# Performance work log

Hardware: AMD Instinct MI355X
Metric: run time of the kernel (lower is better)

The kernel has to match this reference:

```python
import jax, jax.numpy as jnp
import numpy as np

S = 2048   # seq_len
E = 1024   # embed_dim
N = 16     # num_heads
H = 64     # head_dim
CL = 1024  # context_length (sliding window)
BASE = 10000.0


def _rope(x, positions, base=BASE):
    # x: (seq, heads, head_dim); even/odd interleaved rotation per RotaryEmbedding
    hd = x.shape[-1]
    dim = hd // 2
    freqs = jnp.exp(-jnp.arange(dim, dtype=x.dtype) * (np.log(base) / dim))
    angles = positions.astype(x.dtype)[:, None] * freqs[None, :]  # (seq, dim)
    cos = jnp.cos(angles)[:, None, :]
    sin = jnp.sin(angles)[:, None, :]
    xe = x[..., ::2]
    xo = x[..., 1::2]
    re = xe * cos - xo * sin
    ro = xe * sin + xo * cos
    return jnp.zeros_like(x).at[..., ::2].set(re).at[..., 1::2].set(ro)


def setup_inputs() -> dict:
    key = jax.random.key(0)
    ks = jax.random.split(key, 9)
    scale = 1.0 / np.sqrt(E)  # keep logits O(1) like eqx.nn.Linear init
    x = jax.random.normal(ks[0], (S, E), jnp.float32)
    Wq = jax.random.normal(ks[1], (E, E), jnp.float32) * scale
    Wk = jax.random.normal(ks[2], (E, E), jnp.float32) * scale
    Wv = jax.random.normal(ks[3], (E, E), jnp.float32) * scale
    Wo = jax.random.normal(ks[4], (E, E), jnp.float32) * scale
    bq = jax.random.normal(ks[5], (E,), jnp.float32) * 0.01
    bk = jax.random.normal(ks[6], (E,), jnp.float32) * 0.01
    bv = jax.random.normal(ks[7], (E,), jnp.float32) * 0.01
    bo = jax.random.normal(ks[8], (E,), jnp.float32) * 0.01
    k_cache = jnp.zeros((CL - 1, N, H), jnp.float32)
    v_cache = jnp.zeros((CL - 1, N, H), jnp.float32)
    return {"x": x, "Wq": Wq, "bq": bq, "Wk": Wk, "bk": bk, "Wv": Wv,
            "bv": bv, "Wo": Wo, "bo": bo, "k_cache": k_cache,
            "v_cache": v_cache, "position": 0}


def reference(x, Wq, bq, Wk, bk, Wv, bv, Wo, bo, k_cache, v_cache, position):
    seq, emb = x.shape
    clm1, n, h = k_cache.shape  # context_length - 1
    cl = clm1 + 1
    # QKV projections (eqx.nn.Linear: W @ x + b, weight is (out, in))
    q = (x @ Wq.T + bq).reshape(seq, n, h)
    k = (x @ Wk.T + bk).reshape(seq, n, h)
    v = (x @ Wv.T + bv).reshape(seq, n, h)
    # RoPE offset by cache position
    pos = jnp.arange(seq) + position
    q = _rope(q, pos)
    k = _rope(k, pos)
    # Append to cache
    k = jnp.concatenate([k_cache, k], axis=0)  # (seq + cl - 1, n, h)
    v = jnp.concatenate([v_cache, v], axis=0)
    # Sliding-window + causal mask, exactly as SelfAttentionBlock.init_mask
    in_dim = seq + clm1
    m = jnp.tril(jnp.ones((in_dim, seq)))
    neg = 1.0 - jnp.tril(jnp.ones((in_dim, seq)), -cl)
    mask = (m * neg).astype(bool).T  # (seq_q, kv_len)
    # Masked SDPA (same math as jax.nn.dot_product_attention with bool mask)
    scores = jnp.einsum('qnh,knh->nqk', q, k) / jnp.sqrt(jnp.asarray(h, q.dtype))
    scores = jnp.where(mask[None], scores, jnp.asarray(-1e30, scores.dtype))
    attn = jax.nn.softmax(scores, axis=-1)
    o = jnp.einsum('nqk,knh->qnh', attn, v).reshape(seq, n * h)
    out = o @ Wo.T + bo
    new_k = k[-(cl - 1):]
    new_v = v[-(cl - 1):]
    return (out, new_k, new_v)
```

## Files before the change

kernel.cpp:

```cpp
#include <hip/hip_runtime.h>
#include <hip/hip_bf16.h>
#include <stdint.h>

#define SQ   2048
#define EMB  1024
#define NH   16
#define HD   64
#define CLM1 1023
#define KTOT 3071
#define KR   3136

typedef __attribute__((ext_vector_type(8))) short short8;
typedef __attribute__((ext_vector_type(4))) float f32x4;

__device__ __forceinline__ short bf16s(float f) {
  __hip_bfloat16 h = __float2bfloat16(f);
  return *reinterpret_cast<short*>(&h);
}

__device__ __forceinline__ float fexp2(float x) {
  float r;
  asm("v_exp_f32 %0, %1" : "=v"(r) : "v"(x));
  return r;
}

#define GLOAD16(g, l) __builtin_amdgcn_global_load_lds( \
    (const __attribute__((address_space(1))) void*)(g), \
    (__attribute__((address_space(3))) void*)(l), 16, 0, 0)

__global__ __launch_bounds__(256) void k_prep(const float* __restrict__ x,
                                              const float* __restrict__ Wq,
                                              const float* __restrict__ Wk,
                                              const float* __restrict__ Wv,
                                              const float* __restrict__ Wo,
                                              const float* __restrict__ bq,
                                              const float* __restrict__ bk,
                                              const float* __restrict__ bv,
                                              const float* __restrict__ kc,
                                              const int* __restrict__ pos,
                                              short* __restrict__ xb,
                                              short* __restrict__ wqkvb,
                                              short* __restrict__ wob,
                                              float* __restrict__ bqkv,
                                              short* __restrict__ Kc,
                                              float* __restrict__ tabc,
                                              float* __restrict__ tabs) {
  const int b = blockIdx.x;
  const int tid = threadIdx.x;
  if (b < 2048) {
    int i = b * 256 + tid;
    float4 v = ((const float4*)x)[i];
    short4 o; o.x = bf16s(v.x); o.y = bf16s(v.y); o.z = bf16s(v.z); o.w = bf16s(v.w);
    ((short4*)xb)[i] = o;
  } else if (b < 5120) {
    int i = (b - 2048) * 256 + tid;
    int seg = i >> 18;
    int loc = i & 262143;
    const float* W = (seg == 0) ? Wq : (seg == 1) ? Wk : Wv;
    float4 v = ((const float4*)W)[loc];
    short4 o; o.x = bf16s(v.x); o.y = bf16s(v.y); o.z = bf16s(v.z); o.w = bf16s(v.w);
    ((short4*)wqkvb)[i] = o;
  } else if (b < 6144) {
    int i = (b - 5120) * 256 + tid;
    float4 v = ((const float4*)Wo)[i];
    short4 o; o.x = bf16s(v.x); o.y = bf16s(v.y); o.z = bf16s(v.z); o.w = bf16s(v.w);
    ((short4*)wob)[i] = o;
  } else if (b < 10236) {
    int idx = (b - 6144) * 256 + tid;
    int h = idx & 63;
    int n = (idx >> 6) & 15;
    int i = idx >> 10;
    Kc[((size_t)n * KR + i) * HD + h] = bf16s(kc[idx]);
  } else if (b < 10248) {
    int i = (b - 10236) * 256 + tid;
    if (i < 3 * EMB) {
      float v = (i < EMB) ? bq[i] : (i < 2 * EMB) ? bk[i - EMB] : bv[i - 2 * EMB];
      bqkv[i] = v;
    }
  } else {
    int idx = (b - 10248) * 256 + tid;
    int d = idx >> 11;
    int j = idx & 2047;
    float fr = expf(-(float)d * 0.28782313662425575f);
    float ang = (float)(j + pos[0]) * fr;
    float s, c;
    sincosf(ang, &s, &c);
    tabc[d * SQ + j] = c;
    tabs[d * SQ + j] = s;
  }
}

__global__ __launch_bounds__(256) void k_gemmQKV(const short* __restrict__ A,
                                                 const short* __restrict__ B,
                                                 const float* __restrict__ bias,
                                                 const float* __restrict__ tabc,
                                                 const float* __restrict__ tabs,
                                                 short* __restrict__ qbuf,
                                                 short* __restrict__ Kc,
                                                 short* __restrict__ vrows,
                                                 float* __restrict__ nk,
                                                 float* __restrict__ nv) {
  __shared__ short As[4][128 * 32];
  __shared__ short Bs[4][128 * 32];
  const int K = EMB;
  const int tid = threadIdx.x;
  const int lane = tid & 63;
  const int wid = tid >> 6;
  const int wr = wid >> 1, wc = wid & 1;
  const int row0 = blockIdx.x * 128, col0 = blockIdx.y * 128;
  const int lr = lane & 15;
  const int lq = lane >> 4;
  const int lk = lq * 8;
  const int sr = tid >> 2;
  const int sc = (tid & 3) * 8;
  const short* Ag = A + (size_t)(row0 + sr) * K + sc;
  const short* Bg = B + (size_t)(col0 + sr) * K + sc;

  f32x4 acc[4][4] = {};

#define GSTAGE(k0_, b_) { \
    GLOAD16(Ag + (k0_),                  &As[b_][tid * 8]); \
    GLOAD16(Ag + (size_t)64 * K + (k0_), &As[b_][2048 + tid * 8]); \
    GLOAD16(Bg + (k0_),                  &Bs[b_][tid * 8]); \
    GLOAD16(Bg + (size_t)64 * K + (k0_), &Bs[b_][2048 + tid * 8]); }

  const int nkk = K >> 5;
  GSTAGE(0, 0);
  GSTAGE(32, 1);
  for (int ki = 0; ki < nkk; ++ki) {
    int kp = (ki + 2 < nkk) ? ki + 2 : nkk - 1;
    GSTAGE(kp * 32, (ki + 2) & 3);
    asm volatile("s_waitcnt vmcnt(8)" ::: "memory");
    __builtin_amdgcn_s_barrier();
    const short* Ab = As[ki & 3];
    const short* Bb = Bs[ki & 3];
    short8 a[4], bfr[4];
#pragma unroll
    for (int m = 0; m < 4; ++m)
      a[m] = *(const short8*)&Ab[(wr * 64 + m * 16 + lr) * 32 + lk];
#pragma unroll
    for (int nn = 0; nn < 4; ++nn)
      bfr[nn] = *(const short8*)&Bb[(wc * 64 + nn * 16 + lr) * 32 + lk];
#pragma unroll
    for (int m = 0; m < 4; ++m)
#pragma unroll
      for (int nn = 0; nn < 4; ++nn)
        acc[m][nn] = __builtin_amdgcn_mfma_f32_16x16x32_bf16(a[m], bfr[nn], acc[m][nn], 0, 0, 0);
  }
#undef GSTAGE

  const int cseg = col0 >> 10;
#pragma unroll
  for (int m = 0; m < 4; ++m) {
    const int rbase = row0 + wr * 64 + m * 16 + lq * 4;
#pragma unroll
    for (int nn = 0; nn < 4; ++nn) {
      const int cl = wc * 64 + nn * 16 + lr;
      const int c = col0 + cl;
      const float bv = bias[c];
      float v[4];
#pragma unroll
      for (int j = 0; j < 4; ++j) v[j] = acc[m][nn][j] + bv;
      if (cseg < 2) {
        const int d = (cl >> 1) & 31;
        const float4 cs4 = *(const float4*)&tabc[d * SQ + rbase];
        const float4 sn4 = *(const float4*)&tabs[d * SQ + rbase];
        const float cs[4] = {cs4.x, cs4.y, cs4.z, cs4.w};
        const float sn[4] = {sn4.x, sn4.y, sn4.z, sn4.w};
        const bool odd = (c & 1);
        float out[4];
#pragma unroll
        for (int j = 0; j < 4; ++j) {
          float part = __shfl_xor(v[j], 1);
          out[j] = odd ? fmaf(part, sn[j], v[j] * cs[j])
                       : fmaf(part, -sn[j], v[j] * cs[j]);
        }
        const int n = (c >> 6) & 15;
        const int h = c & 63;
        if (cseg == 0) {
#pragma unroll
          for (int j = 0; j < 4; ++j)
            qbuf[((size_t)n * SQ + rbase + j) * HD + h] = bf16s(out[j]);
        } else {
#pragma unroll
          for (int j = 0; j < 4; ++j) {
            Kc[((size_t)n * KR + CLM1 + rbase + j) * HD + h] = bf16s(out[j]);
            if (rbase + j >= 1025)
              nk[((size_t)(rbase + j - 1025) * NH + n) * HD + h] = out[j];
          }
        }
      } else {
        const int cv = c - 2048;
#pragma unroll
        for (int j = 0; j < 4; ++j) {
          vrows[(size_t)(rbase + j) * EMB + cv] = bf16s(v[j]);
          if (rbase + j >= 1025)
            nv[(size_t)(rbase + j - 1025) * EMB + cv] = v[j];
        }
      }
    }
  }
}

__global__ __launch_bounds__(256) void k_vt(const float* __restrict__ vc,
                                            const short* __restrict__ vrows,
                                            short* __restrict__ Vt) {
  const int n = blockIdx.y;
  const int i0 = blockIdx.x * 64;
  const int tid = threadIdx.x;
  __shared__ short T[64][66];
  const int h = tid & 63;
  const int iq = tid >> 6;
#pragma unroll
  for (int e = 0; e < 16; ++e) {
    int il = iq + 4 * e;
    int i = i0 + il;
    short s;
    if (i < CLM1)      s = bf16s(vc[((size_t)i * NH + n) * HD + h]);
    else if (i < KTOT) s = vrows[(size_t)(i - CLM1) * EMB + n * HD + h];
    else               s = 0;
    T[il][h] = s;
  }
  __syncthreads();
  const int h2 = tid >> 2;
  const int c0 = (tid & 3) * 16;
  short* dst = &Vt[((size_t)n * HD + h2) * KR + i0 + c0];
#pragma unroll
  for (int c = 0; c < 2; ++c) {
    short8 o;
#pragma unroll
    for (int e = 0; e < 8; ++e) o[e] = T[c0 + c * 8 + e][h2];
    *(short8*)&dst[c * 8] = o;
  }
}

__global__ __launch_bounds__(256) void k_gemmO(const short* __restrict__ A,
                                               const short* __restrict__ B,
                                               const float* __restrict__ bias,
                                               float* __restrict__ C,
                                               int M, int N, int K) {
  __shared__ short As[4][64 * 32];
  __shared__ short Bs[4][128 * 32];
  const int tid = threadIdx.x;
  const int lane = tid & 63;
  const int wid = tid >> 6;
  const int wr = wid >> 1, wc = wid & 1;
  const int row0 = blockIdx.x * 64, col0 = blockIdx.y * 128;
  const int lr = lane & 15;
  const int lk = (lane >> 4) * 8;
  const int sr = tid >> 2;
  const int sc = (tid & 3) * 8;
  const short* Ag = A + (size_t)(row0 + sr) * K + sc;
  const short* Bg = B + (size_t)(col0 + sr) * K + sc;

  f32x4 acc[2][4] = {};

#define GSTAGEO(k0_, b_) { \
    GLOAD16(Ag + (k0_),                  &As[b_][tid * 8]); \
    GLOAD16(Bg + (k0_),                  &Bs[b_][tid * 8]); \
    GLOAD16(Bg + (size_t)64 * K + (k0_), &Bs[b_][2048 + tid * 8]); }

  const int nk = K >> 5;
  GSTAGEO(0, 0);
  GSTAGEO(32, 1);
  for (int ki = 0; ki < nk; ++ki) {
    int kp = (ki + 2 < nk) ? ki + 2 : nk - 1;
    GSTAGEO(kp * 32, (ki + 2) & 3);
    asm volatile("s_waitcnt vmcnt(6)" ::: "memory");
    __builtin_amdgcn_s_barrier();
    const short* Ab = As[ki & 3];
    const short* Bb = Bs[ki & 3];
    short8 a[2], bfr[4];
#pragma unroll
    for (int m = 0; m < 2; ++m)
      a[m] = *(const short8*)&Ab[(wr * 32 + m * 16 + lr) * 32 + lk];
#pragma unroll
    for (int nn = 0; nn < 4; ++nn)
      bfr[nn] = *(const short8*)&Bb[(wc * 64 + nn * 16 + lr) * 32 + lk];
#pragma unroll
    for (int m = 0; m < 2; ++m)
#pragma unroll
      for (int nn = 0; nn < 4; ++nn)
        acc[m][nn] = __builtin_amdgcn_mfma_f32_16x16x32_bf16(a[m], bfr[nn], acc[m][nn], 0, 0, 0);
  }
#undef GSTAGEO

#pragma unroll
  for (int m = 0; m < 2; ++m) {
    int r = row0 + wr * 32 + m * 16 + (lane >> 4) * 4;
#pragma unroll
    for (int nn = 0; nn < 4; ++nn) {
      int c = col0 + wc * 64 + nn * 16 + lr;
      float bv = bias[c];
#pragma unroll
      for (int j = 0; j < 4; ++j)
        C[(size_t)(r + j) * N + c] = acc[m][nn][j] + bv;
    }
  }
}

__global__ __launch_bounds__(256) void k_attn(const short* __restrict__ qb,
                                              const short* __restrict__ Kc,
                                              const short* __restrict__ Vt,
                                              short* __restrict__ ob) {
  const int bid = blockIdx.x;
  const int hi = bid >> 8;
  const int rr = bid & 255;
  const int n = ((rr & 7) << 1) | hi;
  const int q0 = (rr >> 3) * 64;
  const int tid = threadIdx.x;
  const int wid = tid >> 6;
  const int lane = tid & 63;
  const int lr = lane & 15;
  const int lq = lane >> 4;
  const int lk = lq * 8;
  const int qw = q0 + wid * 16;

  __shared__ short Ks[4][32 * 64];
  __shared__ short Vs[4][64 * 32];
  __shared__ short Pl[4][16][40];

  const short* Qh = qb + (size_t)n * SQ * HD;
  const short* Kh = Kc + (size_t)n * KR * HD;
  const short* Vh = Vt + (size_t)n * HD * KR;

  const int skey = tid >> 3;
  const int ksrc = ((tid & 7) ^ (skey & 7)) << 3;
  const int vh = tid >> 2;
  const int vsrc = ((tid & 3) ^ ((vh >> 1) & 3)) << 3;

  short8 qf0 = *(const short8*)&Qh[(qw + lr) * HD + lk];
  short8 qf1 = *(const short8*)&Qh[(qw + lr) * HD + 32 + lk];

  f32x4 o0 = {0,0,0,0}, o1 = {0,0,0,0}, o2 = {0,0,0,0}, o3 = {0,0,0,0};
  f32x4 ps = {0,0,0,0};
  const float C1 = 0.125f * 1.44269504f;
  const float C2 = -14.0f * 1.44269504f;

  const int kslotA = ((lq ^ (lr & 7)) << 3);
  const int kslotB = (((4 ^ lq) ^ (lr & 7)) << 3);
  const int vslot = ((lq ^ ((lr >> 1) & 3)) << 3);

#define ASTAGE(tt, b_) { int kt_ = q0 + (tt) * 32; \
    GLOAD16(&Kh[(size_t)(kt_ + skey) * HD + ksrc], &Ks[b_][tid * 8]); \
    GLOAD16(&Vh[(size_t)vh * KR + kt_ + vsrc],     &Vs[b_][tid * 8]); }

  ASTAGE(0, 0);
  ASTAGE(1, 1);
  for (int t = 0; t < 34; ++t) {
    int tp = (t + 2 < 34) ? t + 2 : 33;
    ASTAGE(tp, (t + 2) & 3);
    asm volatile("s_waitcnt vmcnt(4)" ::: "memory");
    __builtin_amdgcn_s_barrier();
    const int kt = q0 + t * 32;
    const bool active = (kt + 31 >= qw) && (kt <= qw + 1038);
    if (active) {
      const short* K0 = Ks[t & 3];
      short8 kf0 = *(const short8*)&K0[lr * 64 + kslotA];
      short8 kf1 = *(const short8*)&K0[lr * 64 + kslotB];
      short8 kf2 = *(const short8*)&K0[(16 + lr) * 64 + kslotA];
      short8 kf3 = *(const short8*)&K0[(16 + lr) * 64 + kslotB];
      f32x4 s0 = {0,0,0,0}, s1 = {0,0,0,0};
      s0 = __builtin_amdgcn_mfma_f32_16x16x32_bf16(qf0, kf0, s0, 0, 0, 0);
      s0 = __builtin_amdgcn_mfma_f32_16x16x32_bf16(qf1, kf1, s0, 0, 0, 0);
      s1 = __builtin_amdgcn_mfma_f32_16x16x32_bf16(qf0, kf2, s1, 0, 0, 0);
      s1 = __builtin_amdgcn_mfma_f32_16x16x32_bf16(qf1, kf3, s1, 0, 0, 0);

      float p0[4], p1[4];
      const bool interior = (kt >= qw + 15) && (kt + 31 <= qw + 1023);
      if (interior) {
#pragma unroll
        for (int r = 0; r < 4; ++r) {
          p0[r] = fexp2(fmaf(s0[r], C1, C2));
          p1[r] = fexp2(fmaf(s1[r], C1, C2));
        }
      } else {
        const int key0 = kt + lr, key1 = kt + 16 + lr;
#pragma unroll
        for (int r = 0; r < 4; ++r) {
          int qj = qw + lq * 4 + r;
          float v0 = (key0 >= qj && key0 <= qj + 1023) ? s0[r] : -1e30f;
          float v1 = (key1 >= qj && key1 <= qj + 1023) ? s1[r] : -1e30f;
          p0[r] = fexp2(fmaf(v0, C1, C2));
          p1[r] = fexp2(fmaf(v1, C1, C2));
        }
      }
#pragma unroll
      for (int r = 0; r < 4; ++r) {
        ps[r] += p0[r] + p1[r];
        int prow = lq * 4 + r;
        Pl[wid][prow][lr] = bf16s(p0[r]);
        Pl[wid][prow][lr + 16] = bf16s(p1[r]);
      }
      asm volatile("s_waitcnt lgkmcnt(0)" ::: "memory");
      short8 pf = *(const short8*)&Pl[wid][lr][lk];
      const short* V0 = Vs[t & 3];
      o0 = __builtin_amdgcn_mfma_f32_16x16x32_bf16(pf, *(const short8*)&V0[(0 * 16 + lr) * 32 + vslot], o0, 0, 0, 0);
      o1 = __builtin_amdgcn_mfma_f32_16x16x32_bf16(pf, *(const short8*)&V0[(1 * 16 + lr) * 32 + vslot], o1, 0, 0, 0);
      o2 = __builtin_amdgcn_mfma_f32_16x16x32_bf16(pf, *(const short8*)&V0[(2 * 16 + lr) * 32 + vslot], o2, 0, 0, 0);
      o3 = __builtin_amdgcn_mfma_f32_16x16x32_bf16(pf, *(const short8*)&V0[(3 * 16 + lr) * 32 + vslot], o3, 0, 0, 0);
    }
  }
#undef ASTAGE

#pragma unroll
  for (int r = 0; r < 4; ++r) {
    float rs = ps[r];
    rs += __shfl_xor(rs, 1);
    rs += __shfl_xor(rs, 2);
    rs += __shfl_xor(rs, 4);
    rs += __shfl_xor(rs, 8);
    float inv = 1.0f / rs;
    int qj = qw + lq * 4 + r;
    size_t rowoff = (size_t)qj * EMB + n * HD;
    ob[rowoff + 0 * 16 + lr] = bf16s(o0[r] * inv);
    ob[rowoff + 1 * 16 + lr] = bf16s(o1[r] * inv);
    ob[rowoff + 2 * 16 + lr] = bf16s(o2[r] * inv);
    ob[rowoff + 3 * 16 + lr] = bf16s(o3[r] * inv);
  }
}

extern "C" void kernel_launch(void* const* d_in, const int* in_sizes, int n_in,
                              void* d_out, int out_size, void* d_ws, size_t ws_size,
                              hipStream_t stream) {
  const float* x      = (const float*)d_in[0];
  const float* Wq     = (const float*)d_in[1];
  const float* bq     = (const float*)d_in[2];
  const float* Wk     = (const float*)d_in[3];
  const float* bk     = (const float*)d_in[4];
  const float* Wv     = (const float*)d_in[5];
  const float* bv     = (const float*)d_in[6];
  const float* Wo     = (const float*)d_in[7];
  const float* bo     = (const float*)d_in[8];
  const float* kcache = (const float*)d_in[9];
  const float* vcache = (const float*)d_in[10];
  const int*   pos    = (const int*)d_in[11];

  float* out = (float*)d_out;
  float* nk  = out + (size_t)SQ * EMB;
  float* nv  = nk + (size_t)CLM1 * NH * HD;

  char* w = (char*)d_ws;
  size_t o0 = 0;
  short* xb    = (short*)(w + o0); o0 += (size_t)SQ * EMB * 2;
  short* wqkvb = (short*)(w + o0); o0 += (size_t)3 * EMB * EMB * 2;
  short* wob   = (short*)(w + o0); o0 += (size_t)EMB * EMB * 2;
  float* bqkv  = (float*)(w + o0); o0 += (size_t)3 * EMB * 4;
  float* tabc  = (float*)(w + o0); o0 += (size_t)32 * SQ * 4;
  float* tabs  = (float*)(w + o0); o0 += (size_t)32 * SQ * 4;
  short* qbuf  = (short*)(w + o0); o0 += (size_t)NH * SQ * HD * 2;
  short* Kc    = (short*)(w + o0); o0 += (size_t)NH * KR * HD * 2;
  short* vrows = (short*)(w + o0); o0 += (size_t)SQ * EMB * 2;
  short* Vt    = (short*)(w + o0); o0 += (size_t)NH * HD * KR * 2;
  short* ob    = (short*)(w + o0); o0 += (size_t)SQ * EMB * 2;

  k_prep<<<10504, 256, 0, stream>>>(x, Wq, Wk, Wv, Wo, bq, bk, bv, kcache, pos,
                                    xb, wqkvb, wob, bqkv, Kc, tabc, tabs);
  k_gemmQKV<<<dim3(SQ / 128, 3 * EMB / 128), 256, 0, stream>>>(
      xb, wqkvb, bqkv, tabc, tabs, qbuf, Kc, vrows, nk, nv);
  k_vt<<<dim3(48, NH), 256, 0, stream>>>(vcache, vrows, Vt);
  k_attn<<<512, 256, 0, stream>>>(qbuf, Kc, Vt, ob);
  k_gemmO<<<dim3(SQ / 64, EMB / 128), 256, 0, stream>>>(ob, wob, bo, out, SQ, EMB, EMB);
}
```

Measured before the change: 177.6 us.

## Split attention KV range across two blocks and combine partials

The attention kernel's 34-tile key loop is split into two halves, each handled by a separate block, doubling the grid to 1024 blocks. Each half writes unnormalized fp32 partial outputs and row sums to workspace, and a new combine kernel adds them, normalizes and writes bf16. This works because softmax uses a fixed max offset, so no rescaling is needed. The aim is more parallelism and better CU occupancy, at the cost of an extra launch and about 17 MB of fp32 partial traffic.

Measured after the change: 173.8 us. -2.1%, faster.

```diff
diff --git a/kernel.cpp b/kernel.cpp
--- a/kernel.cpp
+++ b/kernel.cpp
@@ -302,12 +302,16 @@
 __global__ __launch_bounds__(256) void k_attn(const short* __restrict__ qb,
                                               const short* __restrict__ Kc,
                                               const short* __restrict__ Vt,
-                                              short* __restrict__ ob) {
+                                              float* __restrict__ Op,
+                                              float* __restrict__ pss) {
   const int bid = blockIdx.x;
-  const int hi = bid >> 8;
-  const int rr = bid & 255;
+  const int s = bid >> 9;
+  const int low = bid & 511;
+  const int hi = low >> 8;
+  const int rr = low & 255;
   const int n = ((rr & 7) << 1) | hi;
   const int q0 = (rr >> 3) * 64;
+  const int tb = s * 17;
   const int tid = threadIdx.x;
   const int wid = tid >> 6;
   const int lane = tid & 63;
@@ -341,18 +345,18 @@
   const int kslotB = (((4 ^ lq) ^ (lr & 7)) << 3);
   const int vslot = ((lq ^ ((lr >> 1) & 3)) << 3);
 
-#define ASTAGE(tt, b_) { int kt_ = q0 + (tt) * 32; \
+#define ASTAGE(tt, b_) { int kt_ = q0 + (tb + (tt)) * 32; \
     GLOAD16(&Kh[(size_t)(kt_ + skey) * HD + ksrc], &Ks[b_][tid * 8]); \
     GLOAD16(&Vh[(size_t)vh * KR + kt_ + vsrc],     &Vs[b_][tid * 8]); }
 
   ASTAGE(0, 0);
   ASTAGE(1, 1);
-  for (int t = 0; t < 34; ++t) {
-    int tp = (t + 2 < 34) ? t + 2 : 33;
+  for (int t = 0; t < 17; ++t) {
+    int tp = (t + 2 < 17) ? t + 2 : 16;
     ASTAGE(tp, (t + 2) & 3);
     asm volatile("s_waitcnt vmcnt(4)" ::: "memory");
     __builtin_amdgcn_s_barrier();
-    const int kt = q0 + t * 32;
+    const int kt = q0 + (tb + t) * 32;
     const bool active = (kt + 31 >= qw) && (kt <= qw + 1038);
     if (active) {
       const short* K0 = Ks[t & 3];
@@ -403,6 +407,7 @@
   }
 #undef ASTAGE
 
+  const size_t base = ((size_t)(s * NH + n) * SQ);
 #pragma unroll
   for (int r = 0; r < 4; ++r) {
     float rs = ps[r];
@@ -410,14 +415,35 @@
     rs += __shfl_xor(rs, 2);
     rs += __shfl_xor(rs, 4);
     rs += __shfl_xor(rs, 8);
-    float inv = 1.0f / rs;
     int qj = qw + lq * 4 + r;
-    size_t rowoff = (size_t)qj * EMB + n * HD;
-    ob[rowoff + 0 * 16 + lr] = bf16s(o0[r] * inv);
-    ob[rowoff + 1 * 16 + lr] = bf16s(o1[r] * inv);
-    ob[rowoff + 2 * 16 + lr] = bf16s(o2[r] * inv);
-    ob[rowoff + 3 * 16 + lr] = bf16s(o3[r] * inv);
-  }
+    if (lr == 0) pss[base + qj] = rs;
+    float* op = Op + (base + qj) * HD;
+    op[0 * 16 + lr] = o0[r];
+    op[1 * 16 + lr] = o1[r];
+    op[2 * 16 + lr] = o2[r];
+    op[3 * 16 + lr] = o3[r];
+  }
+}
+
+__global__ __launch_bounds__(256) void k_comb(const float* __restrict__ Op,
+                                              const float* __restrict__ pss,
+                                              short* __restrict__ ob) {
+  const int flat = blockIdx.x * 256 + threadIdx.x;
+  const int n = flat >> 15;
+  const int rem = flat & 32767;
+  const int q = rem >> 4;
+  const int h0 = (rem & 15) << 2;
+  const size_t b0 = ((size_t)n * SQ + q);
+  const size_t b1 = ((size_t)(NH + n) * SQ + q);
+  float4 a = *(const float4*)&Op[b0 * HD + h0];
+  float4 b = *(const float4*)&Op[b1 * HD + h0];
+  float inv = 1.0f / (pss[b0] + pss[b1]);
+  short4 o;
+  o.x = bf16s((a.x + b.x) * inv);
+  o.y = bf16s((a.y + b.y) * inv);
+  o.z = bf16s((a.z + b.z) * inv);
+  o.w = bf16s((a.w + b.w) * inv);
+  *(short4*)&ob[(size_t)q * EMB + n * HD + h0] = o;
 }
 
 extern "C" void kernel_launch(void* const* d_in, const int* in_sizes, int n_in,
@@ -453,12 +479,15 @@
   short* vrows = (short*)(w + o0); o0 += (size_t)SQ * EMB * 2;
   short* Vt    = (short*)(w + o0); o0 += (size_t)NH * HD * KR * 2;
   short* ob    = (short*)(w + o0); o0 += (size_t)SQ * EMB * 2;
+  float* Op    = (float*)(w + o0); o0 += (size_t)2 * NH * SQ * HD * 4;
+  float* pss   = (float*)(w + o0); o0 += (size_t)2 * NH * SQ * 4;
 
   k_prep<<<10504, 256, 0, stream>>>(x, Wq, Wk, Wv, Wo, bq, bk, bv, kcache, pos,
                                     xb, wqkvb, wob, bqkv, Kc, tabc, tabs);
   k_gemmQKV<<<dim3(SQ / 128, 3 * EMB / 128), 256, 0, stream>>>(
       xb, wqkvb, bqkv, tabc, tabs, qbuf, Kc, vrows, nk, nv);
   k_vt<<<dim3(48, NH), 256, 0, stream>>>(vcache, vrows, Vt);
-  k_attn<<<512, 256, 0, stream>>>(qbuf, Kc, Vt, ob);
+  k_attn<<<1024, 256, 0, stream>>>(qbuf, Kc, Vt, Op, pss);
+  k_comb<<<2048, 256, 0, stream>>>(Op, pss, ob);
   k_gemmO<<<dim3(SQ / 64, EMB / 128), 256, 0, stream>>>(ob, wob, bo, out, SQ, EMB, EMB);
 }
```
